# Optimization experiments

Measured on AMD Instinct MI355X. Metric: run time of the kernel, lower is better.

The kernel has to match this reference:

```python
import jax, jax.numpy as jnp
import numpy as np
from math import sqrt

IN_DIM = 512
OUT_DIM = 512
MOD_DIM = 256
BATCH = 1024
EPS = 1e-8


def _uniform_param(key, shape, fan_in):
    # torch.rand in [0,1) then scaled to [-k, k) with k = sqrt(1/fan_in)
    k = sqrt(1.0 / fan_in)
    return jax.random.uniform(key, shape, dtype=jnp.float32, minval=-k, maxval=k)


def setup_inputs() -> dict:
    key = jax.random.key(0)
    k1, k2, k3, k4, k5, k6 = jax.random.split(key, 6)
    modulations = jax.random.normal(k1, (BATCH, MOD_DIM), dtype=jnp.float32)
    x = jax.random.normal(k2, (BATCH, IN_DIM), dtype=jnp.float32)
    weight = _uniform_param(k3, (OUT_DIM, IN_DIM), IN_DIM)      # main weight
    bias = _uniform_param(k4, (OUT_DIM,), IN_DIM)               # main bias
    # nn.Linear(modulation_dim, in_dim): weight [in_dim, mod_dim], bias [in_dim]
    mod_w = _uniform_param(k5, (IN_DIM, MOD_DIM), MOD_DIM)
    mod_b = _uniform_param(k6, (IN_DIM,), MOD_DIM)
    return {"modulations": modulations, "x": x, "weight": weight,
            "bias": bias, "mod_w": mod_w, "mod_b": mod_b}


def reference(modulations, x, weight, bias, mod_w, mod_b):
    # scales: [B, in_dim]
    scales = modulations @ mod_w.T + mod_b
    # weight_1: [B, out_dim, in_dim] = weight broadcast-scaled per sample
    w1 = weight[None, :, :] * scales[:, None, :]
    # NOTE: faithful to source: sum over axis -2 (the OUT dim), per-column L2 renorm
    w2 = w1 * jax.lax.rsqrt(jnp.sum(jnp.square(w1), axis=-2, keepdims=True) + EPS)
    # (x.unsqueeze(-2) @ w2.transpose(-2,-1)).squeeze(-2) + bias -> [B, out_dim]
    out = jnp.einsum("bi,boi->bo", x, w2) + bias
    return out
```

## Files before the change

kernel.cpp:

```cpp
#include <hip/hip_runtime.h>
#include <math.h>

#define B_DIM    1024
#define IN_DIMS  512
#define OUT_DIMS 512
#define MOD_DIM  256
#define EPS_F    1e-8f

typedef __attribute__((ext_vector_type(8))) short bf16x8;
typedef __attribute__((ext_vector_type(4))) float f32x4;

__device__ __forceinline__ unsigned short f2bf(float f) {
    union { float f; unsigned u; } c; c.f = f;
    unsigned r = c.u + 0x7fffu + ((c.u >> 16) & 1u);
    return (unsigned short)(r >> 16);
}
__device__ __forceinline__ float bf2f(unsigned short h) {
    union { float f; unsigned u; } c; c.u = ((unsigned)h) << 16;
    return c.f;
}

#define LP1 264
__global__ __launch_bounds__(256) void k1_mod(
    const float* __restrict__ mods,
    const float* __restrict__ mod_w,
    const float* __restrict__ mod_b,
    const float* __restrict__ weight,
    const float* __restrict__ x,
    unsigned short* __restrict__ t_bf)
{
    __shared__ unsigned short Ah[32 * LP1], Al[32 * LP1];
    __shared__ unsigned short Bh[64 * LP1], Bl[64 * LP1];
    __shared__ float4 csm[16][16];
    __shared__ float colsum_s[64];

    const int tid = threadIdx.x;
    const int n0 = blockIdx.x * 64;
    const int m0 = blockIdx.y * 32;
    const int lane = tid & 63, wv = tid >> 6;
    const int wm = (wv >> 1) * 16, wn = (wv & 1) * 32;
    const int lr = lane & 15, lq = lane >> 4;

    #pragma unroll
    for (int i = 0; i < 8; i++) {
        const int id = tid + i * 256;
        const int r = id >> 6, c4 = id & 63;
        float4 v = *(const float4*)&mods[(m0 + r) * MOD_DIM + c4 * 4];
        ushort4 h, l;
        h.x = f2bf(v.x); l.x = f2bf(v.x - bf2f(h.x));
        h.y = f2bf(v.y); l.y = f2bf(v.y - bf2f(h.y));
        h.z = f2bf(v.z); l.z = f2bf(v.z - bf2f(h.z));
        h.w = f2bf(v.w); l.w = f2bf(v.w - bf2f(h.w));
        *(ushort4*)&Ah[r * LP1 + c4 * 4] = h;
        *(ushort4*)&Al[r * LP1 + c4 * 4] = l;
    }
    #pragma unroll
    for (int i = 0; i < 16; i++) {
        const int id = tid + i * 256;
        const int r = id >> 6, c4 = id & 63;
        float4 v = *(const float4*)&mod_w[(n0 + r) * MOD_DIM + c4 * 4];
        ushort4 h, l;
        h.x = f2bf(v.x); l.x = f2bf(v.x - bf2f(h.x));
        h.y = f2bf(v.y); l.y = f2bf(v.y - bf2f(h.y));
        h.z = f2bf(v.z); l.z = f2bf(v.z - bf2f(h.z));
        h.w = f2bf(v.w); l.w = f2bf(v.w - bf2f(h.w));
        *(ushort4*)&Bh[r * LP1 + c4 * 4] = h;
        *(ushort4*)&Bl[r * LP1 + c4 * 4] = l;
    }

    {
        const int c4 = tid & 15, rr = tid >> 4;
        float4 acc = {0.f, 0.f, 0.f, 0.f};
        #pragma unroll
        for (int it = 0; it < 32; it++) {
            const int row = rr + 16 * it;
            float4 v = *(const float4*)&weight[row * IN_DIMS + n0 + c4 * 4];
            acc.x += v.x * v.x; acc.y += v.y * v.y;
            acc.z += v.z * v.z; acc.w += v.w * v.w;
        }
        csm[rr][c4] = acc;
    }
    __syncthreads();
    if (tid < 16) {
        float4 s = csm[0][tid];
        #pragma unroll
        for (int j = 1; j < 16; j++) {
            float4 v = csm[j][tid];
            s.x += v.x; s.y += v.y; s.z += v.z; s.w += v.w;
        }
        *(float4*)&colsum_s[tid * 4] = s;
    }

    f32x4 acc[2] = {};
    #pragma unroll
    for (int kk = 0; kk < 256; kk += 32) {
        const int ko = kk + lq * 8;
        bf16x8 ah = *(bf16x8*)&Ah[(wm + lr) * LP1 + ko];
        bf16x8 al = *(bf16x8*)&Al[(wm + lr) * LP1 + ko];
        bf16x8 bh0 = *(bf16x8*)&Bh[(wn +      lr) * LP1 + ko];
        bf16x8 bh1 = *(bf16x8*)&Bh[(wn + 16 + lr) * LP1 + ko];
        bf16x8 bl0 = *(bf16x8*)&Bl[(wn +      lr) * LP1 + ko];
        bf16x8 bl1 = *(bf16x8*)&Bl[(wn + 16 + lr) * LP1 + ko];
        acc[0] = __builtin_amdgcn_mfma_f32_16x16x32_bf16(ah, bh0, acc[0], 0, 0, 0);
        acc[1] = __builtin_amdgcn_mfma_f32_16x16x32_bf16(ah, bh1, acc[1], 0, 0, 0);
        acc[0] = __builtin_amdgcn_mfma_f32_16x16x32_bf16(ah, bl0, acc[0], 0, 0, 0);
        acc[1] = __builtin_amdgcn_mfma_f32_16x16x32_bf16(ah, bl1, acc[1], 0, 0, 0);
        acc[0] = __builtin_amdgcn_mfma_f32_16x16x32_bf16(al, bh0, acc[0], 0, 0, 0);
        acc[1] = __builtin_amdgcn_mfma_f32_16x16x32_bf16(al, bh1, acc[1], 0, 0, 0);
    }
    __syncthreads();

    #pragma unroll
    for (int j = 0; j < 2; j++) {
        const int ln = wn + 16 * j + lr;
        const int gn = n0 + ln;
        const float cs = colsum_s[ln];
        const float mb = mod_b[gn];
        #pragma unroll
        for (int rr = 0; rr < 4; rr++) {
            const int gm = m0 + wm + lq * 4 + rr;
            const float s = acc[j][rr] + mb;
            const float tv = x[gm * IN_DIMS + gn] * s * rsqrtf(s * s * cs + EPS_F);
            t_bf[gm * IN_DIMS + gn] = f2bf(tv);
        }
    }
}

#define LP2 536
__global__ __launch_bounds__(256) void k2_out(
    const unsigned short* __restrict__ t_bf,
    const float* __restrict__ weight,
    const float* __restrict__ bias,
    float* __restrict__ out)
{
    __shared__ unsigned short As[32 * LP2];
    __shared__ unsigned short Bs[64 * LP2];

    const int tid = threadIdx.x;
    const int n0 = blockIdx.x * 64;
    const int m0 = blockIdx.y * 32;
    const int lane = tid & 63, wv = tid >> 6;
    const int wm = (wv >> 1) * 16, wn = (wv & 1) * 32;
    const int lr = lane & 15, lq = lane >> 4;

    #pragma unroll
    for (int i = 0; i < 8; i++) {
        const int id = tid + i * 256;
        const int r = id >> 6, c8 = id & 63;
        *(uint4*)&As[r * LP2 + c8 * 8] =
            *(const uint4*)&t_bf[(m0 + r) * IN_DIMS + c8 * 8];
    }
    #pragma unroll
    for (int i = 0; i < 32; i++) {
        const int id = tid + i * 256;
        const int r = id >> 7, c4 = id & 127;
        float4 v = *(const float4*)&weight[(n0 + r) * IN_DIMS + c4 * 4];
        ushort4 h;
        h.x = f2bf(v.x); h.y = f2bf(v.y); h.z = f2bf(v.z); h.w = f2bf(v.w);
        *(ushort4*)&Bs[r * LP2 + c4 * 4] = h;
    }
    __syncthreads();

    f32x4 acc[2] = {};
    #pragma unroll
    for (int kk = 0; kk < 512; kk += 32) {
        const int ko = kk + lq * 8;
        bf16x8 a  = *(bf16x8*)&As[(wm + lr) * LP2 + ko];
        bf16x8 b0 = *(bf16x8*)&Bs[(wn +      lr) * LP2 + ko];
        bf16x8 b1 = *(bf16x8*)&Bs[(wn + 16 + lr) * LP2 + ko];
        acc[0] = __builtin_amdgcn_mfma_f32_16x16x32_bf16(a, b0, acc[0], 0, 0, 0);
        acc[1] = __builtin_amdgcn_mfma_f32_16x16x32_bf16(a, b1, acc[1], 0, 0, 0);
    }

    #pragma unroll
    for (int j = 0; j < 2; j++) {
        const int gn = n0 + wn + 16 * j + lr;
        const float bv = bias[gn];
        #pragma unroll
        for (int rr = 0; rr < 4; rr++) {
            const int gm = m0 + wm + lq * 4 + rr;
            out[gm * OUT_DIMS + gn] = acc[j][rr] + bv;
        }
    }
}

extern "C" void kernel_launch(void* const* d_in, const int* in_sizes, int n_in,
                              void* d_out, int out_size, void* d_ws, size_t ws_size,
                              hipStream_t stream)
{
    const float* modulations = (const float*)d_in[0];
    const float* x           = (const float*)d_in[1];
    const float* weight      = (const float*)d_in[2];
    const float* bias        = (const float*)d_in[3];
    const float* mod_w       = (const float*)d_in[4];
    const float* mod_b       = (const float*)d_in[5];
    float* out = (float*)d_out;

    unsigned short* t_bf = (unsigned short*)d_ws;

    k1_mod<<<dim3(8, 32), 256, 0, stream>>>(
        modulations, mod_w, mod_b, weight, x, t_bf);

    k2_out<<<dim3(8, 32), 256, 0, stream>>>(
        t_bf, weight, bias, out);
}
```

Before: 78.04 us.

## Fuse both stages into one kernel with atomic row/column dependency barriers

Merges the modulation/scale kernel and the output GEMM into a single launch. Blocks publish completion through per-row and per-column atomic counters and spin-wait before the second GEMM. The weight is converted to bf16 once, cooperatively, into workspace, and the second stage loads tiles with direct global-to-LDS loads. This removes a kernel launch gap and the redundant per-block weight conversion, but adds a memset launch and relies on all 256 blocks being co-resident for the spin barrier (guarded by an iteration cap).

```diff
diff --git a/kernel.cpp b/kernel.cpp
--- a/kernel.cpp
+++ b/kernel.cpp
@@ -20,23 +20,46 @@
     return c.f;
 }
 
+__device__ __forceinline__ void gload_lds16(const void* g, void* l) {
+    __builtin_amdgcn_global_load_lds(
+        (const __attribute__((address_space(1))) unsigned int*)g,
+        (__attribute__((address_space(3))) unsigned int*)l, 16, 0, 0);
+}
+
 #define LP1 264
-__global__ __launch_bounds__(256) void k1_mod(
+#define LP2 536
+
+__global__ __launch_bounds__(256) void fused(
     const float* __restrict__ mods,
     const float* __restrict__ mod_w,
     const float* __restrict__ mod_b,
     const float* __restrict__ weight,
     const float* __restrict__ x,
-    unsigned short* __restrict__ t_bf)
+    const float* __restrict__ bias,
+    unsigned short* __restrict__ t_bf,
+    unsigned short* __restrict__ wbf,
+    int* __restrict__ cnts,
+    float* __restrict__ out)
 {
-    __shared__ unsigned short Ah[32 * LP1], Al[32 * LP1];
-    __shared__ unsigned short Bh[64 * LP1], Bl[64 * LP1];
-    __shared__ float4 csm[16][16];
-    __shared__ float colsum_s[64];
+    __shared__ union SMem {
+        struct {
+            unsigned short Ah[32 * LP1];
+            unsigned short Al[32 * LP1];
+            unsigned short Bh[64 * LP1];
+            unsigned short Bl[64 * LP1];
+            float4 csm[16][16];
+            float colsum[64];
+        } p1;
+        struct {
+            unsigned short As[32 * LP2];
+            unsigned short Bs[64 * LP2];
+        } p2;
+    } sm;
 
     const int tid = threadIdx.x;
-    const int n0 = blockIdx.x * 64;
-    const int m0 = blockIdx.y * 32;
+    const int bx = blockIdx.x, by = blockIdx.y;
+    const int n0 = bx * 64;
+    const int m0 = by * 32;
     const int lane = tid & 63, wv = tid >> 6;
     const int wm = (wv >> 1) * 16, wn = (wv & 1) * 32;
     const int lr = lane & 15, lq = lane >> 4;
@@ -51,8 +74,8 @@
         h.y = f2bf(v.y); l.y = f2bf(v.y - bf2f(h.y));
         h.z = f2bf(v.z); l.z = f2bf(v.z - bf2f(h.z));
         h.w = f2bf(v.w); l.w = f2bf(v.w - bf2f(h.w));
-        *(ushort4*)&Ah[r * LP1 + c4 * 4] = h;
-        *(ushort4*)&Al[r * LP1 + c4 * 4] = l;
+        *(ushort4*)&sm.p1.Ah[r * LP1 + c4 * 4] = h;
+        *(ushort4*)&sm.p1.Al[r * LP1 + c4 * 4] = l;
     }
     #pragma unroll
     for (int i = 0; i < 16; i++) {
@@ -64,8 +87,28 @@
         h.y = f2bf(v.y); l.y = f2bf(v.y - bf2f(h.y));
         h.z = f2bf(v.z); l.z = f2bf(v.z - bf2f(h.z));
         h.w = f2bf(v.w); l.w = f2bf(v.w - bf2f(h.w));
-        *(ushort4*)&Bh[r * LP1 + c4 * 4] = h;
-        *(ushort4*)&Bl[r * LP1 + c4 * 4] = l;
+        *(ushort4*)&sm.p1.Bh[r * LP1 + c4 * 4] = h;
+        *(ushort4*)&sm.p1.Bl[r * LP1 + c4 * 4] = l;
+    }
+
+    {
+        const int row = n0 + by * 2 + (tid >> 7);
+        const int c4 = tid & 127;
+        float4 v = *(const float4*)&weight[row * IN_DIMS + c4 * 4];
+        ushort4 h;
+        h.x = f2bf(v.x); h.y = f2bf(v.y); h.z = f2bf(v.z); h.w = f2bf(v.w);
+        *(ushort4*)&wbf[row * IN_DIMS + c4 * 4] = h;
+    }
+
+    float xv[2][4];
+    #pragma unroll
+    for (int j = 0; j < 2; j++) {
+        const int gn = n0 + wn + 16 * j + lr;
+        #pragma unroll
+        for (int rr = 0; rr < 4; rr++) {
+            const int gm = m0 + wm + lq * 4 + rr;
+            xv[j][rr] = x[gm * IN_DIMS + gn];
+        }
     }
 
     {
@@ -78,29 +121,29 @@
             acc.x += v.x * v.x; acc.y += v.y * v.y;
             acc.z += v.z * v.z; acc.w += v.w * v.w;
         }
-        csm[rr][c4] = acc;
+        sm.p1.csm[rr][c4] = acc;
     }
     __syncthreads();
     if (tid < 16) {
-        float4 s = csm[0][tid];
+        float4 s = sm.p1.csm[0][tid];
         #pragma unroll
         for (int j = 1; j < 16; j++) {
-            float4 v = csm[j][tid];
+            float4 v = sm.p1.csm[j][tid];
             s.x += v.x; s.y += v.y; s.z += v.z; s.w += v.w;
         }
-        *(float4*)&colsum_s[tid * 4] = s;
+        *(float4*)&sm.p1.colsum[tid * 4] = s;
     }
 
     f32x4 acc[2] = {};
     #pragma unroll
     for (int kk = 0; kk < 256; kk += 32) {
         const int ko = kk + lq * 8;
-        bf16x8 ah = *(bf16x8*)&Ah[(wm + lr) * LP1 + ko];
-        bf16x8 al = *(bf16x8*)&Al[(wm + lr) * LP1 + ko];
-        bf16x8 bh0 = *(bf16x8*)&Bh[(wn +      lr) * LP1 + ko];
-        bf16x8 bh1 = *(bf16x8*)&Bh[(wn + 16 + lr) * LP1 + ko];
-        bf16x8 bl0 = *(bf16x8*)&Bl[(wn +      lr) * LP1 + ko];
-        bf16x8 bl1 = *(bf16x8*)&Bl[(wn + 16 + lr) * LP1 + ko];
+        bf16x8 ah = *(bf16x8*)&sm.p1.Ah[(wm + lr) * LP1 + ko];
+        bf16x8 al = *(bf16x8*)&sm.p1.Al[(wm + lr) * LP1 + ko];
+        bf16x8 bh0 = *(bf16x8*)&sm.p1.Bh[(wn +      lr) * LP1 + ko];
+        bf16x8 bh1 = *(bf16x8*)&sm.p1.Bh[(wn + 16 + lr) * LP1 + ko];
+        bf16x8 bl0 = *(bf16x8*)&sm.p1.Bl[(wn +      lr) * LP1 + ko];
+        bf16x8 bl1 = *(bf16x8*)&sm.p1.Bl[(wn + 16 + lr) * LP1 + ko];
         acc[0] = __builtin_amdgcn_mfma_f32_16x16x32_bf16(ah, bh0, acc[0], 0, 0, 0);
         acc[1] = __builtin_amdgcn_mfma_f32_16x16x32_bf16(ah, bh1, acc[1], 0, 0, 0);
         acc[0] = __builtin_amdgcn_mfma_f32_16x16x32_bf16(ah, bl0, acc[0], 0, 0, 0);
@@ -114,72 +157,72 @@
     for (int j = 0; j < 2; j++) {
         const int ln = wn + 16 * j + lr;
         const int gn = n0 + ln;
-        const float cs = colsum_s[ln];
+        const float cs = sm.p1.colsum[ln];
         const float mb = mod_b[gn];
         #pragma unroll
         for (int rr = 0; rr < 4; rr++) {
             const int gm = m0 + wm + lq * 4 + rr;
             const float s = acc[j][rr] + mb;
-            const float tv = x[gm * IN_DIMS + gn] * s * rsqrtf(s * s * cs + EPS_F);
+            const float tv = xv[j][rr] * s * rsqrtf(s * s * cs + EPS_F);
             t_bf[gm * IN_DIMS + gn] = f2bf(tv);
         }
     }
-}
-
-#define LP2 536
-__global__ __launch_bounds__(256) void k2_out(
-    const unsigned short* __restrict__ t_bf,
-    const float* __restrict__ weight,
-    const float* __restrict__ bias,
-    float* __restrict__ out)
-{
-    __shared__ unsigned short As[32 * LP2];
-    __shared__ unsigned short Bs[64 * LP2];
-
-    const int tid = threadIdx.x;
-    const int n0 = blockIdx.x * 64;
-    const int m0 = blockIdx.y * 32;
-    const int lane = tid & 63, wv = tid >> 6;
-    const int wm = (wv >> 1) * 16, wn = (wv & 1) * 32;
-    const int lr = lane & 15, lq = lane >> 4;
+
+    __syncthreads();
+    if (tid == 0) {
+        __threadfence();
+        __hip_atomic_fetch_add(&cnts[by], 1,
+                               __ATOMIC_RELEASE, __HIP_MEMORY_SCOPE_AGENT);
+        __hip_atomic_fetch_add(&cnts[32 + bx], 1,
+                               __ATOMIC_RELEASE, __HIP_MEMORY_SCOPE_AGENT);
+        int guard = 0;
+        while (guard < 300000) {
+            int yv = __hip_atomic_load(&cnts[by],
+                                       __ATOMIC_RELAXED, __HIP_MEMORY_SCOPE_AGENT);
+            int xvv = __hip_atomic_load(&cnts[32 + bx],
+                                        __ATOMIC_RELAXED, __HIP_MEMORY_SCOPE_AGENT);
+            if (yv >= 8 && xvv >= 32) break;
+            __builtin_amdgcn_s_sleep(2);
+            guard++;
+        }
+    }
+    __syncthreads();
+    __threadfence();
+
+    const float bv0 = bias[n0 + wn + lr];
+    const float bv1 = bias[n0 + wn + 16 + lr];
 
     #pragma unroll
     for (int i = 0; i < 8; i++) {
-        const int id = tid + i * 256;
-        const int r = id >> 6, c8 = id & 63;
-        *(uint4*)&As[r * LP2 + c8 * 8] =
-            *(const uint4*)&t_bf[(m0 + r) * IN_DIMS + c8 * 8];
-    }
-    #pragma unroll
-    for (int i = 0; i < 32; i++) {
-        const int id = tid + i * 256;
-        const int r = id >> 7, c4 = id & 127;
-        float4 v = *(const float4*)&weight[(n0 + r) * IN_DIMS + c4 * 4];
-        ushort4 h;
-        h.x = f2bf(v.x); h.y = f2bf(v.y); h.z = f2bf(v.z); h.w = f2bf(v.w);
-        *(ushort4*)&Bs[r * LP2 + c4 * 4] = h;
-    }
-    __syncthreads();
-
-    f32x4 acc[2] = {};
+        const int r = wv * 8 + i;
+        gload_lds16(t_bf + (m0 + r) * IN_DIMS + lane * 8, &sm.p2.As[r * LP2]);
+    }
+    #pragma unroll
+    for (int i = 0; i < 16; i++) {
+        const int r = wv * 16 + i;
+        gload_lds16(wbf + (n0 + r) * IN_DIMS + lane * 8, &sm.p2.Bs[r * LP2]);
+    }
+    __syncthreads();
+
+    f32x4 acc2[2] = {};
     #pragma unroll
     for (int kk = 0; kk < 512; kk += 32) {
         const int ko = kk + lq * 8;
-        bf16x8 a  = *(bf16x8*)&As[(wm + lr) * LP2 + ko];
-        bf16x8 b0 = *(bf16x8*)&Bs[(wn +      lr) * LP2 + ko];
-        bf16x8 b1 = *(bf16x8*)&Bs[(wn + 16 + lr) * LP2 + ko];
-        acc[0] = __builtin_amdgcn_mfma_f32_16x16x32_bf16(a, b0, acc[0], 0, 0, 0);
-        acc[1] = __builtin_amdgcn_mfma_f32_16x16x32_bf16(a, b1, acc[1], 0, 0, 0);
+        bf16x8 a  = *(bf16x8*)&sm.p2.As[(wm + lr) * LP2 + ko];
+        bf16x8 b0 = *(bf16x8*)&sm.p2.Bs[(wn +      lr) * LP2 + ko];
+        bf16x8 b1 = *(bf16x8*)&sm.p2.Bs[(wn + 16 + lr) * LP2 + ko];
+        acc2[0] = __builtin_amdgcn_mfma_f32_16x16x32_bf16(a, b0, acc2[0], 0, 0, 0);
+        acc2[1] = __builtin_amdgcn_mfma_f32_16x16x32_bf16(a, b1, acc2[1], 0, 0, 0);
     }
 
     #pragma unroll
     for (int j = 0; j < 2; j++) {
         const int gn = n0 + wn + 16 * j + lr;
-        const float bv = bias[gn];
+        const float bvv = j ? bv1 : bv0;
         #pragma unroll
         for (int rr = 0; rr < 4; rr++) {
             const int gm = m0 + wm + lq * 4 + rr;
-            out[gm * OUT_DIMS + gn] = acc[j][rr] + bv;
+            out[gm * OUT_DIMS + gn] = acc2[j][rr] + bvv;
         }
     }
 }
@@ -197,10 +240,11 @@
     float* out = (float*)d_out;
 
     unsigned short* t_bf = (unsigned short*)d_ws;
-
-    k1_mod<<<dim3(8, 32), 256, 0, stream>>>(
-        modulations, mod_w, mod_b, weight, x, t_bf);
-
-    k2_out<<<dim3(8, 32), 256, 0, stream>>>(
-        t_bf, weight, bias, out);
-}
+    unsigned short* wbf  = (unsigned short*)d_ws + (1024 * 512);
+    int* cnts = (int*)((char*)d_ws + (4 << 20));
+
+    hipMemsetAsync(cnts, 0, 256, stream);
+
+    fused<<<dim3(8, 32), 256, 0, stream>>>(
+        modulations, mod_w, mod_b, weight, x, bias, t_bf, wbf, cnts, out);
+}
```

New measurement: 104.4 us. 33.7% more time.

## Pre-convert weight to bf16 in k1, load via global_load_lds, use 512 threads

Applied to the files above, without the earlier changes.

k1 now converts the main weight to bf16 and writes it to workspace, with each block handling two rows. This lets k2 read half as many bytes and skip the per-block fp32-to-bf16 conversion. k2 fills its LDS tiles with direct global-to-LDS loads, and both kernels move to 8 waves per block with one 16x16 MFMA tile per wave. The x loads in k1 are also hoisted ahead of the GEMM. The cost is an extra bf16 weight write in k1 and a larger workspace.

```diff
diff --git a/kernel.cpp b/kernel.cpp
--- a/kernel.cpp
+++ b/kernel.cpp
@@ -20,30 +20,37 @@
     return c.f;
 }
 
+__device__ __forceinline__ void gload_lds16(const void* g, void* l) {
+    __builtin_amdgcn_global_load_lds(
+        (const __attribute__((address_space(1))) unsigned int*)g,
+        (__attribute__((address_space(3))) unsigned int*)l, 16, 0, 0);
+}
+
 #define LP1 264
-__global__ __launch_bounds__(256) void k1_mod(
+__global__ __launch_bounds__(512) void k1_mod(
     const float* __restrict__ mods,
     const float* __restrict__ mod_w,
     const float* __restrict__ mod_b,
     const float* __restrict__ weight,
     const float* __restrict__ x,
-    unsigned short* __restrict__ t_bf)
+    unsigned short* __restrict__ t_bf,
+    unsigned short* __restrict__ wbf)
 {
     __shared__ unsigned short Ah[32 * LP1], Al[32 * LP1];
     __shared__ unsigned short Bh[64 * LP1], Bl[64 * LP1];
-    __shared__ float4 csm[16][16];
+    __shared__ float4 csm[32][16];
     __shared__ float colsum_s[64];
 
     const int tid = threadIdx.x;
     const int n0 = blockIdx.x * 64;
     const int m0 = blockIdx.y * 32;
     const int lane = tid & 63, wv = tid >> 6;
-    const int wm = (wv >> 1) * 16, wn = (wv & 1) * 32;
+    const int wm = (wv >> 2) * 16, wn = (wv & 3) * 16;
     const int lr = lane & 15, lq = lane >> 4;
 
     #pragma unroll
-    for (int i = 0; i < 8; i++) {
-        const int id = tid + i * 256;
+    for (int i = 0; i < 4; i++) {
+        const int id = tid + i * 512;
         const int r = id >> 6, c4 = id & 63;
         float4 v = *(const float4*)&mods[(m0 + r) * MOD_DIM + c4 * 4];
         ushort4 h, l;
@@ -55,8 +62,8 @@
         *(ushort4*)&Al[r * LP1 + c4 * 4] = l;
     }
     #pragma unroll
-    for (int i = 0; i < 16; i++) {
-        const int id = tid + i * 256;
+    for (int i = 0; i < 8; i++) {
+        const int id = tid + i * 512;
         const int r = id >> 6, c4 = id & 63;
         float4 v = *(const float4*)&mod_w[(n0 + r) * MOD_DIM + c4 * 4];
         ushort4 h, l;
@@ -68,12 +75,31 @@
         *(ushort4*)&Bl[r * LP1 + c4 * 4] = l;
     }
 
+    if (tid < 256) {
+        const int row = n0 + blockIdx.y * 2 + (tid >> 7);
+        const int c4 = tid & 127;
+        float4 v = *(const float4*)&weight[row * IN_DIMS + c4 * 4];
+        ushort4 h;
+        h.x = f2bf(v.x); h.y = f2bf(v.y); h.z = f2bf(v.z); h.w = f2bf(v.w);
+        *(ushort4*)&wbf[row * IN_DIMS + c4 * 4] = h;
+    }
+
+    float xv[4];
+    {
+        const int gn = n0 + wn + lr;
+        #pragma unroll
+        for (int rr = 0; rr < 4; rr++) {
+            const int gm = m0 + wm + lq * 4 + rr;
+            xv[rr] = x[gm * IN_DIMS + gn];
+        }
+    }
+
     {
         const int c4 = tid & 15, rr = tid >> 4;
         float4 acc = {0.f, 0.f, 0.f, 0.f};
         #pragma unroll
-        for (int it = 0; it < 32; it++) {
-            const int row = rr + 16 * it;
+        for (int it = 0; it < 16; it++) {
+            const int row = rr + 32 * it;
             float4 v = *(const float4*)&weight[row * IN_DIMS + n0 + c4 * 4];
             acc.x += v.x * v.x; acc.y += v.y * v.y;
             acc.z += v.z * v.z; acc.w += v.w * v.w;
@@ -84,52 +110,46 @@
     if (tid < 16) {
         float4 s = csm[0][tid];
         #pragma unroll
-        for (int j = 1; j < 16; j++) {
+        for (int j = 1; j < 32; j++) {
             float4 v = csm[j][tid];
             s.x += v.x; s.y += v.y; s.z += v.z; s.w += v.w;
         }
         *(float4*)&colsum_s[tid * 4] = s;
     }
 
-    f32x4 acc[2] = {};
+    f32x4 acc = {};
     #pragma unroll
     for (int kk = 0; kk < 256; kk += 32) {
         const int ko = kk + lq * 8;
         bf16x8 ah = *(bf16x8*)&Ah[(wm + lr) * LP1 + ko];
         bf16x8 al = *(bf16x8*)&Al[(wm + lr) * LP1 + ko];
-        bf16x8 bh0 = *(bf16x8*)&Bh[(wn +      lr) * LP1 + ko];
-        bf16x8 bh1 = *(bf16x8*)&Bh[(wn + 16 + lr) * LP1 + ko];
-        bf16x8 bl0 = *(bf16x8*)&Bl[(wn +      lr) * LP1 + ko];
-        bf16x8 bl1 = *(bf16x8*)&Bl[(wn + 16 + lr) * LP1 + ko];
-        acc[0] = __builtin_amdgcn_mfma_f32_16x16x32_bf16(ah, bh0, acc[0], 0, 0, 0);
-        acc[1] = __builtin_amdgcn_mfma_f32_16x16x32_bf16(ah, bh1, acc[1], 0, 0, 0);
-        acc[0] = __builtin_amdgcn_mfma_f32_16x16x32_bf16(ah, bl0, acc[0], 0, 0, 0);
-        acc[1] = __builtin_amdgcn_mfma_f32_16x16x32_bf16(ah, bl1, acc[1], 0, 0, 0);
-        acc[0] = __builtin_amdgcn_mfma_f32_16x16x32_bf16(al, bh0, acc[0], 0, 0, 0);
-        acc[1] = __builtin_amdgcn_mfma_f32_16x16x32_bf16(al, bh1, acc[1], 0, 0, 0);
+        bf16x8 bh = *(bf16x8*)&Bh[(wn + lr) * LP1 + ko];
+        bf16x8 bl = *(bf16x8*)&Bl[(wn + lr) * LP1 + ko];
+        acc = __builtin_amdgcn_mfma_f32_16x16x32_bf16(ah, bh, acc, 0, 0, 0);
+        acc = __builtin_amdgcn_mfma_f32_16x16x32_bf16(ah, bl, acc, 0, 0, 0);
+        acc = __builtin_amdgcn_mfma_f32_16x16x32_bf16(al, bh, acc, 0, 0, 0);
     }
     __syncthreads();
 
-    #pragma unroll
-    for (int j = 0; j < 2; j++) {
-        const int ln = wn + 16 * j + lr;
+    {
+        const int ln = wn + lr;
         const int gn = n0 + ln;
         const float cs = colsum_s[ln];
         const float mb = mod_b[gn];
         #pragma unroll
         for (int rr = 0; rr < 4; rr++) {
             const int gm = m0 + wm + lq * 4 + rr;
-            const float s = acc[j][rr] + mb;
-            const float tv = x[gm * IN_DIMS + gn] * s * rsqrtf(s * s * cs + EPS_F);
+            const float s = acc[rr] + mb;
+            const float tv = xv[rr] * s * rsqrtf(s * s * cs + EPS_F);
             t_bf[gm * IN_DIMS + gn] = f2bf(tv);
         }
     }
 }
 
 #define LP2 536
-__global__ __launch_bounds__(256) void k2_out(
+__global__ __launch_bounds__(512) void k2_out(
     const unsigned short* __restrict__ t_bf,
-    const float* __restrict__ weight,
+    const unsigned short* __restrict__ wbf,
     const float* __restrict__ bias,
     float* __restrict__ out)
 {
@@ -140,46 +160,38 @@
     const int n0 = blockIdx.x * 64;
     const int m0 = blockIdx.y * 32;
     const int lane = tid & 63, wv = tid >> 6;
-    const int wm = (wv >> 1) * 16, wn = (wv & 1) * 32;
+    const int wm = (wv >> 2) * 16, wn = (wv & 3) * 16;
     const int lr = lane & 15, lq = lane >> 4;
 
+    const float bv = bias[n0 + wn + lr];
+
+    #pragma unroll
+    for (int i = 0; i < 4; i++) {
+        const int r = wv * 4 + i;
+        gload_lds16(t_bf + (m0 + r) * IN_DIMS + lane * 8, &As[r * LP2]);
+    }
     #pragma unroll
     for (int i = 0; i < 8; i++) {
-        const int id = tid + i * 256;
-        const int r = id >> 6, c8 = id & 63;
-        *(uint4*)&As[r * LP2 + c8 * 8] =
-            *(const uint4*)&t_bf[(m0 + r) * IN_DIMS + c8 * 8];
-    }
-    #pragma unroll
-    for (int i = 0; i < 32; i++) {
-        const int id = tid + i * 256;
-        const int r = id >> 7, c4 = id & 127;
-        float4 v = *(const float4*)&weight[(n0 + r) * IN_DIMS + c4 * 4];
-        ushort4 h;
-        h.x = f2bf(v.x); h.y = f2bf(v.y); h.z = f2bf(v.z); h.w = f2bf(v.w);
-        *(ushort4*)&Bs[r * LP2 + c4 * 4] = h;
+        const int r = wv * 8 + i;
+        gload_lds16(wbf + (n0 + r) * IN_DIMS + lane * 8, &Bs[r * LP2]);
     }
     __syncthreads();
 
-    f32x4 acc[2] = {};
+    f32x4 acc = {};
     #pragma unroll
     for (int kk = 0; kk < 512; kk += 32) {
         const int ko = kk + lq * 8;
-        bf16x8 a  = *(bf16x8*)&As[(wm + lr) * LP2 + ko];
-        bf16x8 b0 = *(bf16x8*)&Bs[(wn +      lr) * LP2 + ko];
-        bf16x8 b1 = *(bf16x8*)&Bs[(wn + 16 + lr) * LP2 + ko];
-        acc[0] = __builtin_amdgcn_mfma_f32_16x16x32_bf16(a, b0, acc[0], 0, 0, 0);
-        acc[1] = __builtin_amdgcn_mfma_f32_16x16x32_bf16(a, b1, acc[1], 0, 0, 0);
-    }
-
-    #pragma unroll
-    for (int j = 0; j < 2; j++) {
-        const int gn = n0 + wn + 16 * j + lr;
-        const float bv = bias[gn];
+        bf16x8 a = *(bf16x8*)&As[(wm + lr) * LP2 + ko];
+        bf16x8 b = *(bf16x8*)&Bs[(wn + lr) * LP2 + ko];
+        acc = __builtin_amdgcn_mfma_f32_16x16x32_bf16(a, b, acc, 0, 0, 0);
+    }
+
+    {
+        const int gn = n0 + wn + lr;
         #pragma unroll
         for (int rr = 0; rr < 4; rr++) {
             const int gm = m0 + wm + lq * 4 + rr;
-            out[gm * OUT_DIMS + gn] = acc[j][rr] + bv;
+            out[gm * OUT_DIMS + gn] = acc[rr] + bv;
         }
     }
 }
@@ -197,10 +209,11 @@
     float* out = (float*)d_out;
 
     unsigned short* t_bf = (unsigned short*)d_ws;
-
-    k1_mod<<<dim3(8, 32), 256, 0, stream>>>(
-        modulations, mod_w, mod_b, weight, x, t_bf);
-
-    k2_out<<<dim3(8, 32), 256, 0, stream>>>(
-        t_bf, weight, bias, out);
-}
+    unsigned short* wbf  = (unsigned short*)d_ws + (1024 * 512);
+
+    k1_mod<<<dim3(8, 32), 512, 0, stream>>>(
+        modulations, mod_w, mod_b, weight, x, t_bf, wbf);
+
+    k2_out<<<dim3(8, 32), 512, 0, stream>>>(
+        t_bf, wbf, bias, out);
+}
```

New measurement: 75.21 us. 3.6% less time.
